# Kernel optimization log

Measured on AMD Instinct MI355X. Metric: run time of the kernel, lower is better.

Reference implementation:

```python
import jax, jax.numpy as jnp
import numpy as np

B, D_IN, H = 32768, 256, 128
N_TASK, N_EXP, N_SHARE = 2, 4, 4


def setup_inputs() -> dict:
    key = jax.random.key(0)
    ks = jax.random.split(key, 4)
    s = 1.0 / np.sqrt(D_IN)
    return {
        "x": jax.random.normal(ks[0], (B, D_IN), dtype=jnp.float32),
        "W_share": jax.random.normal(ks[1], (N_SHARE, D_IN, H), dtype=jnp.float32) * s,
        "b_share": jnp.zeros((N_SHARE, H), dtype=jnp.float32),
        "W_task": jax.random.normal(ks[2], (N_TASK, N_EXP, D_IN, H), dtype=jnp.float32) * s,
        "b_task": jnp.zeros((N_TASK, N_EXP, H), dtype=jnp.float32),
        "W_gate": jax.random.normal(ks[3], (N_TASK, D_IN, N_SHARE + N_EXP), dtype=jnp.float32) * s,
        "b_gate": jnp.zeros((N_TASK, N_SHARE + N_EXP), dtype=jnp.float32),
    }


def reference(x, W_share, b_share, W_task, b_task, W_gate, b_gate):
    # shared experts: [B, N_SHARE, H]
    share = jax.nn.relu(jnp.einsum('bd,edh->beh', x, W_share) + b_share)
    # task-specific experts: [T, B, N_EXP, H]
    task = jax.nn.relu(jnp.einsum('bd,tedh->tbeh', x, W_task) + b_task[:, None])
    # gates: [T, B, N_SHARE + N_EXP], softmax over experts
    gate = jax.nn.softmax(jnp.einsum('bd,tdg->tbg', x, W_gate) + b_gate[:, None], axis=-1)
    # concat order matches original: share_net first, then task experts
    share_b = jnp.broadcast_to(share[None], (N_TASK, B, N_SHARE, H))
    experts = jnp.concatenate([share_b, task], axis=2)  # [T, B, N_SHARE+N_EXP, H]
    towers = jnp.einsum('tbeh,tbe->tbh', experts, gate)  # [T, B, H]
    return towers
```

## Files before the change

kernel.cpp:

```cpp
#include <hip/hip_runtime.h>


typedef __attribute__((ext_vector_type(8))) short short8;
typedef __attribute__((ext_vector_type(4))) float float4v;

#define UNIT_B   18432
#define ROW_B    144
#define WAVE_B   4608
#define WGT_OFF  442368

__device__ __forceinline__ unsigned short f2bf(float f) {
  unsigned u = __builtin_bit_cast(unsigned, f);
  u += 0x7FFFu + ((u >> 16) & 1u);
  return (unsigned short)(u >> 16);
}

__device__ __forceinline__ int slot2e(int sr, int t) {
  return (sr < 4) ? sr : 4 + t * 4 + (sr - 4);
}

__global__ __launch_bounds__(256)
void prep_kernel(const float* __restrict__ Ws,
                 const float* __restrict__ Wt,
                 const float* __restrict__ Wg,
                 unsigned short* __restrict__ WT2) {
  int bid = blockIdx.x;
  int tid = threadIdx.x;
  if (bid < 96) {
    __shared__ float tile[64][65];
    int e  = bid >> 3;
    int kt = (bid >> 1) & 3;
    int ht = bid & 1;
    const float* src = (e < 4) ? Ws + ((size_t)e << 15)
                               : Wt + ((size_t)(e - 4) << 15);
    int m = tid & 15, n = tid >> 4;
    #pragma unroll
    for (int i = 0; i < 4; ++i) {
      int kl = i * 16 + n;
      float4 v = *(const float4*)&src[(size_t)(kt * 64 + kl) * 128 + ht * 64 + m * 4];
      tile[kl][m * 4 + 0] = v.x;
      tile[kl][m * 4 + 1] = v.y;
      tile[kl][m * 4 + 2] = v.z;
      tile[kl][m * 4 + 3] = v.w;
    }
    __syncthreads();
    #pragma unroll
    for (int i = 0; i < 4; ++i) {
      int hl = i * 16 + n;
      size_t base = ((size_t)(e * 4 + kt) * 128 + ht * 64 + hl) * 72;
      ushort4 o;
      o.x = f2bf(tile[m * 4 + 0][hl]);
      o.y = f2bf(tile[m * 4 + 1][hl]);
      o.z = f2bf(tile[m * 4 + 2][hl]);
      o.w = f2bf(tile[m * 4 + 3][hl]);
      *(ushort4*)&WT2[base + m * 4] = o;
      if (m < 2) {
        ushort4 z = {0, 0, 0, 0};
        *(ushort4*)&WT2[base + 64 + m * 4] = z;
      }
    }
  } else {
    unsigned short* WgT = WT2 + WGT_OFF;
    #pragma unroll
    for (int it = 0; it < 16; ++it) {
      int j = it * 256 + tid;
      int n = j >> 8, k = j & 255;
      int t = n >> 3, g = n & 7;
      WgT[j] = f2bf(Wg[(size_t)(t * 256 + k) * 8 + g]);
    }
  }
}

__global__ __launch_bounds__(256, 3)
void dmoe_main(const float* __restrict__ x,
               const unsigned short* __restrict__ WT2,
               const float* __restrict__ b_share,
               const float* __restrict__ b_task,
               const float* __restrict__ b_gate,
               float* __restrict__ out) {
  __shared__ unsigned short Bs0[UNIT_B / 2];
  __shared__ unsigned short Bs1[UNIT_B / 2];
  __shared__ float gates[8 * 68];

  const int tid  = threadIdx.x;
  const int lane = tid & 63;
  const int w    = tid >> 6;
  const int col  = lane & 15;
  const int quad = lane >> 4;
  const int mg   = w & 1;
  const int ng   = w >> 1;
  const int blk  = blockIdx.x;
  const int t    = blk & 1;
  const int rt   = blk >> 1;
  const int rot  = (blk >> 3) & 7;
  const int hb   = ng * 64;

  const char* WT2b = (const char*)WT2;

  const int sr0 = rot;
  const int e0  = slot2e(sr0, t);
  uint4 p0, p1, p2, p3; uint2 p4;
  {
    const char* g = WT2b + (size_t)(e0 * 4 + 0) * UNIT_B + w * WAVE_B;
    p0 = *(const uint4*)(g + lane * 16);
    p1 = *(const uint4*)(g + 1024 + lane * 16);
    p2 = *(const uint4*)(g + 2048 + lane * 16);
    p3 = *(const uint4*)(g + 3072 + lane * 16);
    p4 = *(const uint2*)(g + 4096 + lane * 8);
  }

  short8 A[2][8];
  {
    const float* xb = x + ((size_t)rt * 64 + mg * 32 + col) * 256 + quad * 8;
    #pragma unroll
    for (int mt = 0; mt < 2; ++mt) {
      const float* xr = xb + (size_t)mt * 16 * 256;
      #pragma unroll
      for (int k = 0; k < 8; ++k) {
        float4 u = *(const float4*)(xr + k * 32);
        float4 v = *(const float4*)(xr + k * 32 + 4);
        short8 fr;
        fr[0] = (short)f2bf(u.x); fr[1] = (short)f2bf(u.y);
        fr[2] = (short)f2bf(u.z); fr[3] = (short)f2bf(u.w);
        fr[4] = (short)f2bf(v.x); fr[5] = (short)f2bf(v.y);
        fr[6] = (short)f2bf(v.z); fr[7] = (short)f2bf(v.w);
        A[mt][k] = fr;
      }
    }
  }

  {
    const unsigned short* WgT = WT2 + WGT_OFF;
    int gr = (col < 8) ? col : 7;
    const unsigned short* bp = WgT + (size_t)(t * 8 + gr) * 256 + quad * 8;
    short8 Bg[8];
    #pragma unroll
    for (int k = 0; k < 8; ++k) Bg[k] = *(const short8*)(bp + k * 32);
    float bg = b_gate[t * 8 + gr];
    #pragma unroll
    for (int mt = 0; mt < 2; ++mt) {
      float4v ag = {0.f, 0.f, 0.f, 0.f};
      #pragma unroll
      for (int k = 0; k < 8; ++k)
        ag = __builtin_amdgcn_mfma_f32_16x16x32_bf16(A[mt][k], Bg[k], ag, 0, 0, 0);
      #pragma unroll
      for (int r = 0; r < 4; ++r) {
        float vlog = ag[r] + bg;
        float m = vlog;
        m = fmaxf(m, __shfl_xor(m, 1));
        m = fmaxf(m, __shfl_xor(m, 2));
        m = fmaxf(m, __shfl_xor(m, 4));
        float p = __expf(vlog - m);
        float s = p;
        s += __shfl_xor(s, 1);
        s += __shfl_xor(s, 2);
        s += __shfl_xor(s, 4);
        if (ng == 0 && col < 8)
          gates[col * 68 + mg * 32 + mt * 16 + quad * 4 + r] = p / s;
      }
    }
  }

  {
    char* l = (char*)Bs0 + w * WAVE_B;
    *(uint4*)(l + lane * 16)        = p0;
    *(uint4*)(l + 1024 + lane * 16) = p1;
    *(uint4*)(l + 2048 + lane * 16) = p2;
    *(uint4*)(l + 3072 + lane * 16) = p3;
    *(uint2*)(l + 4096 + lane * 8)  = p4;
  }
  __syncthreads();

  float tw[2][4][4];
  #pragma unroll
  for (int mt = 0; mt < 2; ++mt)
    #pragma unroll
    for (int nt = 0; nt < 4; ++nt)
      #pragma unroll
      for (int r = 0; r < 4; ++r)
        tw[mt][nt][r] = 0.f;

  #pragma unroll 1
  for (int s = 0; s < 8; ++s) {
    const int sr  = (s + rot) & 7;
    const int e   = slot2e(sr, t);
    const int gc  = sr;
    const int sr2 = (s + 1 + rot) & 7;
    const int e2  = slot2e(sr2, t);
    const float* bp = (sr < 4) ? (b_share + sr * 128)
                               : (b_task + (size_t)(t * 4 + (sr - 4)) * 128);
    float bias[4];
    #pragma unroll
    for (int nt = 0; nt < 4; ++nt) bias[nt] = bp[hb + nt * 16 + col];

    float4v acc[2][4];
    #pragma unroll
    for (int mt = 0; mt < 2; ++mt)
      #pragma unroll
      for (int nt = 0; nt < 4; ++nt)
        acc[mt][nt] = (float4v){0.f, 0.f, 0.f, 0.f};

    #pragma unroll
    for (int kq = 0; kq < 4; ++kq) {
      const bool doStage = !(s == 7 && kq == 3);
      const int  en  = (kq < 3) ? e : e2;
      const int  kqn = (kq + 1) & 3;
      uint4 q0, q1, q2, q3; uint2 q4;
      if (doStage) {
        const char* g = WT2b + (size_t)(en * 4 + kqn) * UNIT_B + w * WAVE_B;
        q0 = *(const uint4*)(g + lane * 16);
        q1 = *(const uint4*)(g + 1024 + lane * 16);
        q2 = *(const uint4*)(g + 2048 + lane * 16);
        q3 = *(const uint4*)(g + 3072 + lane * 16);
        q4 = *(const uint2*)(g + 4096 + lane * 8);
      }
      {
        const char* Bb = (const char*)((kq & 1) ? Bs1 : Bs0);
        #pragma unroll
        for (int kk = 0; kk < 2; ++kk) {
          #pragma unroll
          for (int nt = 0; nt < 4; ++nt) {
            short8 bfr = *(const short8*)(Bb + (hb + nt * 16 + col) * ROW_B
                                          + kk * 64 + quad * 16);
            acc[0][nt] = __builtin_amdgcn_mfma_f32_16x16x32_bf16(
                A[0][kq * 2 + kk], bfr, acc[0][nt], 0, 0, 0);
            acc[1][nt] = __builtin_amdgcn_mfma_f32_16x16x32_bf16(
                A[1][kq * 2 + kk], bfr, acc[1][nt], 0, 0, 0);
          }
        }
      }
      if (doStage) {
        char* l = (char*)((kq & 1) ? Bs0 : Bs1) + w * WAVE_B;
        *(uint4*)(l + lane * 16)        = q0;
        *(uint4*)(l + 1024 + lane * 16) = q1;
        *(uint4*)(l + 2048 + lane * 16) = q2;
        *(uint4*)(l + 3072 + lane * 16) = q3;
        *(uint2*)(l + 4096 + lane * 8)  = q4;
      }
      if (kq == 3) {
        #pragma unroll
        for (int mt = 0; mt < 2; ++mt) {
          float4 gv = *(const float4*)&gates[gc * 68 + mg * 32 + mt * 16 + quad * 4];
          #pragma unroll
          for (int nt = 0; nt < 4; ++nt)
            #pragma unroll
            for (int r = 0; r < 4; ++r) {
              float v = fmaxf(acc[mt][nt][r] + bias[nt], 0.f);
              tw[mt][nt][r] += ((const float*)&gv)[r] * v;
            }
        }
      }
      __syncthreads();
    }
  }

  #pragma unroll
  for (int mt = 0; mt < 2; ++mt)
    #pragma unroll
    for (int r = 0; r < 4; ++r) {
      size_t row = (size_t)rt * 64 + mg * 32 + mt * 16 + quad * 4 + r;
      float* op = out + ((size_t)t << 22) + row * 128 + hb;
      #pragma unroll
      for (int nt = 0; nt < 4; ++nt)
        op[nt * 16 + col] = tw[mt][nt][r];
    }
}

extern "C" void kernel_launch(void* const* d_in, const int* in_sizes, int n_in,
                              void* d_out, int out_size, void* d_ws, size_t ws_size,
                              hipStream_t stream) {
  const float* x       = (const float*)d_in[0];
  const float* W_share = (const float*)d_in[1];
  const float* b_share = (const float*)d_in[2];
  const float* W_task  = (const float*)d_in[3];
  const float* b_task  = (const float*)d_in[4];
  const float* W_gate  = (const float*)d_in[5];
  const float* b_gate  = (const float*)d_in[6];
  float* out = (float*)d_out;
  unsigned short* WT2 = (unsigned short*)d_ws;

  prep_kernel<<<97, 256, 0, stream>>>(W_share, W_task, W_gate, WT2);
  dmoe_main<<<1024, 256, 0, stream>>>(x, WT2, b_share, b_task, b_gate, out);
}
```

Baseline: 171.5 us.

## Process both tasks per block, sharing shared-expert GEMMs across tasks

The main kernel now gives each 512-thread block 128 rows and both tasks. The four shared experts are computed once and applied to both towers with their two gate sets, instead of being recomputed per task. Weight staging moves to half-K units of 128 along K with a wider padded row. The weight workspace is replicated up to four times so different blocks read different copies, and biases are staged in LDS. The cost is more registers for two tower accumulators, fewer blocks (256), and a prep kernel that writes several copies.

```diff
diff --git a/kernel.cpp b/kernel.cpp
--- a/kernel.cpp
+++ b/kernel.cpp
@@ -4,10 +4,14 @@
 typedef __attribute__((ext_vector_type(8))) short short8;
 typedef __attribute__((ext_vector_type(4))) float float4v;
 
-#define UNIT_B   18432
-#define ROW_B    144
-#define WAVE_B   4608
-#define WGT_OFF  442368
+#define ROW_US     136
+#define ROW_B      272
+#define UNIT_US    17408
+#define UNIT_B     34816
+#define WAVE_B     4352
+#define WGT_OFF_US 417792
+#define COPY_US    421888
+#define COPY_B     843776
 
 __device__ __forceinline__ unsigned short f2bf(float f) {
   unsigned u = __builtin_bit_cast(unsigned, f);
@@ -15,15 +19,11 @@
   return (unsigned short)(u >> 16);
 }
 
-__device__ __forceinline__ int slot2e(int sr, int t) {
-  return (sr < 4) ? sr : 4 + t * 4 + (sr - 4);
-}
-
 __global__ __launch_bounds__(256)
 void prep_kernel(const float* __restrict__ Ws,
                  const float* __restrict__ Wt,
                  const float* __restrict__ Wg,
-                 unsigned short* __restrict__ WT2) {
+                 unsigned short* __restrict__ WT, int NC) {
   int bid = blockIdx.x;
   int tid = threadIdx.x;
   if (bid < 96) {
@@ -47,71 +47,70 @@
     #pragma unroll
     for (int i = 0; i < 4; ++i) {
       int hl = i * 16 + n;
-      size_t base = ((size_t)(e * 4 + kt) * 128 + ht * 64 + hl) * 72;
       ushort4 o;
       o.x = f2bf(tile[m * 4 + 0][hl]);
       o.y = f2bf(tile[m * 4 + 1][hl]);
       o.z = f2bf(tile[m * 4 + 2][hl]);
       o.w = f2bf(tile[m * 4 + 3][hl]);
-      *(ushort4*)&WT2[base + m * 4] = o;
-      if (m < 2) {
-        ushort4 z = {0, 0, 0, 0};
-        *(ushort4*)&WT2[base + 64 + m * 4] = z;
+      size_t rowbase = (size_t)(e * 2 + (kt >> 1)) * UNIT_US
+                     + (size_t)(ht * 64 + hl) * ROW_US + (kt & 1) * 64;
+      for (int c = 0; c < NC; ++c) {
+        *(ushort4*)&WT[(size_t)c * COPY_US + rowbase + m * 4] = o;
+        if ((kt & 1) == 1 && m < 2) {
+          ushort4 z = {0, 0, 0, 0};
+          *(ushort4*)&WT[(size_t)c * COPY_US + rowbase + 64 + m * 4] = z;
+        }
       }
     }
   } else {
-    unsigned short* WgT = WT2 + WGT_OFF;
     #pragma unroll
     for (int it = 0; it < 16; ++it) {
       int j = it * 256 + tid;
       int n = j >> 8, k = j & 255;
       int t = n >> 3, g = n & 7;
-      WgT[j] = f2bf(Wg[(size_t)(t * 256 + k) * 8 + g]);
+      unsigned short v = f2bf(Wg[(size_t)(t * 256 + k) * 8 + g]);
+      for (int c = 0; c < NC; ++c)
+        WT[(size_t)c * COPY_US + WGT_OFF_US + j] = v;
     }
   }
 }
 
-__global__ __launch_bounds__(256, 3)
+__global__ __launch_bounds__(512, 2)
 void dmoe_main(const float* __restrict__ x,
-               const unsigned short* __restrict__ WT2,
+               const unsigned short* __restrict__ WT,
                const float* __restrict__ b_share,
                const float* __restrict__ b_task,
                const float* __restrict__ b_gate,
-               float* __restrict__ out) {
-  __shared__ unsigned short Bs0[UNIT_B / 2];
-  __shared__ unsigned short Bs1[UNIT_B / 2];
-  __shared__ float gates[8 * 68];
+               float* __restrict__ out, int NC) {
+  __shared__ unsigned short Bs0[UNIT_US];
+  __shared__ unsigned short Bs1[UNIT_US];
+  __shared__ float gatesL[16 * 132];
+  __shared__ float biasLds[12 * 128];
 
   const int tid  = threadIdx.x;
   const int lane = tid & 63;
   const int w    = tid >> 6;
   const int col  = lane & 15;
   const int quad = lane >> 4;
-  const int mg   = w & 1;
-  const int ng   = w >> 1;
+  const int mg   = w >> 1;
+  const int ng   = w & 1;
   const int blk  = blockIdx.x;
-  const int t    = blk & 1;
-  const int rt   = blk >> 1;
-  const int rot  = (blk >> 3) & 7;
-  const int hb   = ng * 64;
-
-  const char* WT2b = (const char*)WT2;
-
-  const int sr0 = rot;
-  const int e0  = slot2e(sr0, t);
-  uint4 p0, p1, p2, p3; uint2 p4;
+
+  const char* WTc = (const char*)WT + (size_t)((blk >> 3) % NC) * COPY_B;
+
+  uint4 p0, p1, p2, p3; unsigned p4;
   {
-    const char* g = WT2b + (size_t)(e0 * 4 + 0) * UNIT_B + w * WAVE_B;
+    const char* g = WTc + w * WAVE_B;
     p0 = *(const uint4*)(g + lane * 16);
     p1 = *(const uint4*)(g + 1024 + lane * 16);
     p2 = *(const uint4*)(g + 2048 + lane * 16);
     p3 = *(const uint4*)(g + 3072 + lane * 16);
-    p4 = *(const uint2*)(g + 4096 + lane * 8);
+    p4 = *(const unsigned*)(g + 4096 + lane * 4);
   }
 
   short8 A[2][8];
   {
-    const float* xb = x + ((size_t)rt * 64 + mg * 32 + col) * 256 + quad * 8;
+    const float* xb = x + ((size_t)blk * 128 + mg * 32 + col) * 256 + quad * 8;
     #pragma unroll
     for (int mt = 0; mt < 2; ++mt) {
       const float* xr = xb + (size_t)mt * 16 * 256;
@@ -129,14 +128,16 @@
     }
   }
 
+  for (int i = tid; i < 1536; i += 512)
+    biasLds[i] = (i < 512) ? b_share[i] : b_task[i - 512];
+
   {
-    const unsigned short* WgT = WT2 + WGT_OFF;
-    int gr = (col < 8) ? col : 7;
-    const unsigned short* bp = WgT + (size_t)(t * 8 + gr) * 256 + quad * 8;
+    const unsigned short* WgT = (const unsigned short*)(WTc + WGT_OFF_US * 2);
+    const unsigned short* bp = WgT + (size_t)col * 256 + quad * 8;
     short8 Bg[8];
     #pragma unroll
     for (int k = 0; k < 8; ++k) Bg[k] = *(const short8*)(bp + k * 32);
-    float bg = b_gate[t * 8 + gr];
+    float bg = b_gate[col];
     #pragma unroll
     for (int mt = 0; mt < 2; ++mt) {
       float4v ag = {0.f, 0.f, 0.f, 0.f};
@@ -155,8 +156,8 @@
         s += __shfl_xor(s, 1);
         s += __shfl_xor(s, 2);
         s += __shfl_xor(s, 4);
-        if (ng == 0 && col < 8)
-          gates[col * 68 + mg * 32 + mt * 16 + quad * 4 + r] = p / s;
+        if (ng == 0)
+          gatesL[col * 132 + mg * 32 + mt * 16 + quad * 4 + r] = p / s;
       }
     }
   }
@@ -167,87 +168,104 @@
     *(uint4*)(l + 1024 + lane * 16) = p1;
     *(uint4*)(l + 2048 + lane * 16) = p2;
     *(uint4*)(l + 3072 + lane * 16) = p3;
-    *(uint2*)(l + 4096 + lane * 8)  = p4;
+    *(unsigned*)(l + 4096 + lane * 4) = p4;
   }
   __syncthreads();
 
-  float tw[2][4][4];
+  float tw[2][2][4][4];
   #pragma unroll
-  for (int mt = 0; mt < 2; ++mt)
-    #pragma unroll
-    for (int nt = 0; nt < 4; ++nt)
-      #pragma unroll
-      for (int r = 0; r < 4; ++r)
-        tw[mt][nt][r] = 0.f;
+  for (int t = 0; t < 2; ++t)
+    #pragma unroll
+    for (int mt = 0; mt < 2; ++mt)
+      #pragma unroll
+      for (int nt = 0; nt < 4; ++nt)
+        #pragma unroll
+        for (int r = 0; r < 4; ++r)
+          tw[t][mt][nt][r] = 0.f;
+
+  const int hb = ng * 64;
+  float4v acc[2][4];
 
   #pragma unroll 1
-  for (int s = 0; s < 8; ++s) {
-    const int sr  = (s + rot) & 7;
-    const int e   = slot2e(sr, t);
-    const int gc  = sr;
-    const int sr2 = (s + 1 + rot) & 7;
-    const int e2  = slot2e(sr2, t);
-    const float* bp = (sr < 4) ? (b_share + sr * 128)
-                               : (b_task + (size_t)(t * 4 + (sr - 4)) * 128);
-    float bias[4];
-    #pragma unroll
-    for (int nt = 0; nt < 4; ++nt) bias[nt] = bp[hb + nt * 16 + col];
-
-    float4v acc[2][4];
-    #pragma unroll
-    for (int mt = 0; mt < 2; ++mt)
-      #pragma unroll
-      for (int nt = 0; nt < 4; ++nt)
-        acc[mt][nt] = (float4v){0.f, 0.f, 0.f, 0.f};
-
-    #pragma unroll
-    for (int kq = 0; kq < 4; ++kq) {
-      const bool doStage = !(s == 7 && kq == 3);
-      const int  en  = (kq < 3) ? e : e2;
-      const int  kqn = (kq + 1) & 3;
-      uint4 q0, q1, q2, q3; uint2 q4;
+  for (int e = 0; e < 12; ++e) {
+    #pragma unroll
+    for (int kh = 0; kh < 2; ++kh) {
+      const int u = e * 2 + kh;
+      uint4 q0, q1, q2, q3; unsigned q4;
+      const bool doStage = (u < 23);
       if (doStage) {
-        const char* g = WT2b + (size_t)(en * 4 + kqn) * UNIT_B + w * WAVE_B;
+        const char* g = WTc + (size_t)(u + 1) * UNIT_B + w * WAVE_B;
         q0 = *(const uint4*)(g + lane * 16);
         q1 = *(const uint4*)(g + 1024 + lane * 16);
         q2 = *(const uint4*)(g + 2048 + lane * 16);
         q3 = *(const uint4*)(g + 3072 + lane * 16);
-        q4 = *(const uint2*)(g + 4096 + lane * 8);
+        q4 = *(const unsigned*)(g + 4096 + lane * 4);
+      }
+      if (kh == 0) {
+        #pragma unroll
+        for (int mt = 0; mt < 2; ++mt)
+          #pragma unroll
+          for (int nt = 0; nt < 4; ++nt)
+            acc[mt][nt] = (float4v){0.f, 0.f, 0.f, 0.f};
       }
       {
-        const char* Bb = (const char*)((kq & 1) ? Bs1 : Bs0);
-        #pragma unroll
-        for (int kk = 0; kk < 2; ++kk) {
+        const char* Bb = (const char*)(kh ? Bs1 : Bs0);
+        #pragma unroll
+        for (int kk = 0; kk < 4; ++kk) {
           #pragma unroll
           for (int nt = 0; nt < 4; ++nt) {
             short8 bfr = *(const short8*)(Bb + (hb + nt * 16 + col) * ROW_B
                                           + kk * 64 + quad * 16);
             acc[0][nt] = __builtin_amdgcn_mfma_f32_16x16x32_bf16(
-                A[0][kq * 2 + kk], bfr, acc[0][nt], 0, 0, 0);
+                A[0][kh * 4 + kk], bfr, acc[0][nt], 0, 0, 0);
             acc[1][nt] = __builtin_amdgcn_mfma_f32_16x16x32_bf16(
-                A[1][kq * 2 + kk], bfr, acc[1][nt], 0, 0, 0);
+                A[1][kh * 4 + kk], bfr, acc[1][nt], 0, 0, 0);
           }
         }
       }
       if (doStage) {
-        char* l = (char*)((kq & 1) ? Bs0 : Bs1) + w * WAVE_B;
+        char* l = (char*)(kh ? Bs0 : Bs1) + w * WAVE_B;
         *(uint4*)(l + lane * 16)        = q0;
         *(uint4*)(l + 1024 + lane * 16) = q1;
         *(uint4*)(l + 2048 + lane * 16) = q2;
         *(uint4*)(l + 3072 + lane * 16) = q3;
-        *(uint2*)(l + 4096 + lane * 8)  = q4;
-      }
-      if (kq == 3) {
-        #pragma unroll
-        for (int mt = 0; mt < 2; ++mt) {
-          float4 gv = *(const float4*)&gates[gc * 68 + mg * 32 + mt * 16 + quad * 4];
+        *(unsigned*)(l + 4096 + lane * 4) = q4;
+      }
+      if (kh == 1) {
+        float bias[4];
+        #pragma unroll
+        for (int nt = 0; nt < 4; ++nt)
+          bias[nt] = biasLds[e * 128 + hb + nt * 16 + col];
+        if (e < 4) {
           #pragma unroll
-          for (int nt = 0; nt < 4; ++nt)
+          for (int mt = 0; mt < 2; ++mt) {
+            int rb = mg * 32 + mt * 16 + quad * 4;
+            float4 g0 = *(const float4*)&gatesL[e * 132 + rb];
+            float4 g1 = *(const float4*)&gatesL[(8 + e) * 132 + rb];
             #pragma unroll
-            for (int r = 0; r < 4; ++r) {
-              float v = fmaxf(acc[mt][nt][r] + bias[nt], 0.f);
-              tw[mt][nt][r] += ((const float*)&gv)[r] * v;
-            }
+            for (int nt = 0; nt < 4; ++nt)
+              #pragma unroll
+              for (int r = 0; r < 4; ++r) {
+                float v = fmaxf(acc[mt][nt][r] + bias[nt], 0.f);
+                tw[0][mt][nt][r] += ((const float*)&g0)[r] * v;
+                tw[1][mt][nt][r] += ((const float*)&g1)[r] * v;
+              }
+          }
+        } else {
+          const int t  = (e - 4) >> 2;
+          const int gc = t * 8 + 4 + ((e - 4) & 3);
+          #pragma unroll
+          for (int mt = 0; mt < 2; ++mt) {
+            int rb = mg * 32 + mt * 16 + quad * 4;
+            float4 g = *(const float4*)&gatesL[gc * 132 + rb];
+            #pragma unroll
+            for (int nt = 0; nt < 4; ++nt)
+              #pragma unroll
+              for (int r = 0; r < 4; ++r) {
+                float v = fmaxf(acc[mt][nt][r] + bias[nt], 0.f);
+                tw[t][mt][nt][r] += ((const float*)&g)[r] * v;
+              }
+          }
         }
       }
       __syncthreads();
@@ -255,15 +273,17 @@
   }
 
   #pragma unroll
-  for (int mt = 0; mt < 2; ++mt)
-    #pragma unroll
-    for (int r = 0; r < 4; ++r) {
-      size_t row = (size_t)rt * 64 + mg * 32 + mt * 16 + quad * 4 + r;
-      float* op = out + ((size_t)t << 22) + row * 128 + hb;
-      #pragma unroll
-      for (int nt = 0; nt < 4; ++nt)
-        op[nt * 16 + col] = tw[mt][nt][r];
-    }
+  for (int t = 0; t < 2; ++t)
+    #pragma unroll
+    for (int mt = 0; mt < 2; ++mt)
+      #pragma unroll
+      for (int r = 0; r < 4; ++r) {
+        size_t row = (size_t)blk * 128 + mg * 32 + mt * 16 + quad * 4 + r;
+        float* op = out + ((size_t)t << 22) + row * 128 + hb;
+        #pragma unroll
+        for (int nt = 0; nt < 4; ++nt)
+          op[nt * 16 + col] = tw[t][mt][nt][r];
+      }
 }
 
 extern "C" void kernel_launch(void* const* d_in, const int* in_sizes, int n_in,
@@ -277,8 +297,12 @@
   const float* W_gate  = (const float*)d_in[5];
   const float* b_gate  = (const float*)d_in[6];
   float* out = (float*)d_out;
-  unsigned short* WT2 = (unsigned short*)d_ws;
-
-  prep_kernel<<<97, 256, 0, stream>>>(W_share, W_task, W_gate, WT2);
-  dmoe_main<<<1024, 256, 0, stream>>>(x, WT2, b_share, b_task, b_gate, out);
+  unsigned short* WT = (unsigned short*)d_ws;
+
+  int NC = (int)(ws_size / (size_t)COPY_B);
+  if (NC < 1) NC = 1;
+  if (NC > 4) NC = 4;
+
+  prep_kernel<<<97, 256, 0, stream>>>(W_share, W_task, W_gate, WT, NC);
+  dmoe_main<<<256, 512, 0, stream>>>(x, WT, b_share, b_task, b_gate, out, NC);
 }
```

New measurement: 191.7 us. +11.7%, slower.
